# Kernel optimization log

Hardware: AMD Instinct MI355X
Metric: run time of the kernel (lower is better)

The kernel has to match this reference:

```python
import jax, jax.numpy as jnp
import numpy as np

EPS = 1e-06


def setup_inputs() -> dict:
    key = jax.random.key(0)
    k_feat, k_gamma, k_beta = jax.random.split(key, 3)
    N, C, B = 1_000_000, 64, 8
    feat = jax.random.normal(k_feat, (N, C), dtype=jnp.float32)
    # cumulative offsets: 8 equal segments of 125k points, last == N
    offset = (jnp.arange(1, B + 1, dtype=jnp.int64)) * (N // B)
    gamma = jax.random.normal(k_gamma, (1, C), dtype=jnp.float32) * 0.1
    beta = jax.random.normal(k_beta, (1, C), dtype=jnp.float32) * 0.1
    return {"feat": feat, "offset": offset, "gamma": gamma, "beta": beta}


def reference(feat, offset, gamma, beta):
    N, C = feat.shape
    B = offset.shape[0]
    # segment id of each point: first offset strictly greater than index
    batch = jnp.searchsorted(offset, jnp.arange(N), side="right")  # [N]
    # per-segment L2 norm over points, per channel: sqrt(sum feat^2)
    sumsq = jax.ops.segment_sum(feat * feat, batch, num_segments=B)  # [B, C]
    response = jnp.sqrt(sumsq)  # [B, C]
    response_norm = response / (jnp.mean(response, axis=1, keepdims=True) + EPS)  # [B, C]
    # broadcast per-segment channel scale back to points
    out = feat + gamma * (feat * response_norm[batch]) + beta  # [N, C]
    return out
```

## Files before the change

kernel.cpp:

```cpp
#include <hip/hip_runtime.h>
#include <math.h>

#define EPS 1e-6f
#define C_CH 64
#define BPS_A 256
#define BPS_C 256

typedef float f32x4 __attribute__((ext_vector_type(4)));

__global__ __launch_bounds__(256) void sumsq_partial(
    const float4* __restrict__ feat,
    const int* __restrict__ offset,
    float* __restrict__ partial)
{
    const int seg  = blockIdx.x / BPS_A;
    const int bip  = blockIdx.x - seg * BPS_A;
    const int start = (seg == 0) ? 0 : offset[seg - 1];
    const int end   = offset[seg];

    const int t    = threadIdx.x;
    const int c4   = t & 15;
    const int rsub = t >> 4;

    float4 a0 = make_float4(0.f, 0.f, 0.f, 0.f);
    float4 a1 = make_float4(0.f, 0.f, 0.f, 0.f);

    const int stride = BPS_A * 32;
    for (int row = start + bip * 32 + rsub; row < end; row += stride) {
        float4 v = feat[row * 16 + c4];
        a0.x = fmaf(v.x, v.x, a0.x);
        a0.y = fmaf(v.y, v.y, a0.y);
        a0.z = fmaf(v.z, v.z, a0.z);
        a0.w = fmaf(v.w, v.w, a0.w);
        int row2 = row + 16;
        if (row2 < end) {
            float4 w = feat[row2 * 16 + c4];
            a1.x = fmaf(w.x, w.x, a1.x);
            a1.y = fmaf(w.y, w.y, a1.y);
            a1.z = fmaf(w.z, w.z, a1.z);
            a1.w = fmaf(w.w, w.w, a1.w);
        }
    }
    a0.x += a1.x; a0.y += a1.y; a0.z += a1.z; a0.w += a1.w;

    __shared__ float lds[16][C_CH];
    lds[rsub][4 * c4 + 0] = a0.x;
    lds[rsub][4 * c4 + 1] = a0.y;
    lds[rsub][4 * c4 + 2] = a0.z;
    lds[rsub][4 * c4 + 3] = a0.w;
    __syncthreads();

    if (t < C_CH) {
        float s = 0.f;
        #pragma unroll
        for (int r = 0; r < 16; ++r) s += lds[r][t];
        partial[blockIdx.x * C_CH + t] = s;
    }
}

__global__ __launch_bounds__(256) void apply_kernel(
    const float4* __restrict__ feat,
    const int* __restrict__ offset,
    const float* __restrict__ partial,
    const float* __restrict__ gamma,
    const float4* __restrict__ beta4,
    f32x4* __restrict__ out)
{
    const int seg = blockIdx.x / BPS_C;
    const int bip = blockIdx.x - seg * BPS_C;
    const int start = (seg == 0) ? 0 : offset[seg - 1];
    const int end   = offset[seg];

    const int t    = threadIdx.x;
    const int c    = t & 63;
    const int q    = t >> 6;

    __shared__ float red[4][C_CH];
    __shared__ float mulsh[C_CH];

    {
        float s = 0.f;
        const float* p = partial + (seg * BPS_A) * C_CH + c;
        for (int b = q; b < BPS_A; b += 4) s += p[b * C_CH];
        red[q][c] = s;
        __syncthreads();
        if (t < C_CH) {
            float tot  = red[0][c] + red[1][c] + red[2][c] + red[3][c];
            float resp = sqrtf(tot);
            float m = resp;
            #pragma unroll
            for (int off = 1; off < 64; off <<= 1) m += __shfl_xor(m, off, 64);
            float mean = m * (1.0f / 64.0f);
            float rn   = resp / (mean + EPS);
            mulsh[c] = 1.0f + gamma[c] * rn;
        }
        __syncthreads();
    }

    const int c4 = t & 15;
    const int rsub = t >> 4;
    const float4 mm = ((const float4*)mulsh)[c4];
    const float4 bt = beta4[c4];

    const int stride = BPS_C * 32;
    for (int row = start + bip * 32 + rsub; row < end; row += stride) {
        float4 v = feat[row * 16 + c4];
        f32x4 o;
        o.x = fmaf(v.x, mm.x, bt.x);
        o.y = fmaf(v.y, mm.y, bt.y);
        o.z = fmaf(v.z, mm.z, bt.z);
        o.w = fmaf(v.w, mm.w, bt.w);
        __builtin_nontemporal_store(o, &out[row * 16 + c4]);
        int row2 = row + 16;
        if (row2 < end) {
            float4 w = feat[row2 * 16 + c4];
            f32x4 o2;
            o2.x = fmaf(w.x, mm.x, bt.x);
            o2.y = fmaf(w.y, mm.y, bt.y);
            o2.z = fmaf(w.z, mm.z, bt.z);
            o2.w = fmaf(w.w, mm.w, bt.w);
            __builtin_nontemporal_store(o2, &out[row2 * 16 + c4]);
        }
    }
}

extern "C" void kernel_launch(void* const* d_in, const int* in_sizes, int n_in,
                              void* d_out, int out_size, void* d_ws, size_t ws_size,
                              hipStream_t stream)
{
    const float4* feat   = (const float4*)d_in[0];
    const int*    offset = (const int*)d_in[1];
    const float*  gamma  = (const float*)d_in[2];
    const float4* beta4  = (const float4*)d_in[3];
    f32x4*        out    = (f32x4*)d_out;

    const int B = in_sizes[1];

    float* partial = (float*)d_ws;

    sumsq_partial<<<B * BPS_A, 256, 0, stream>>>(feat, offset, partial);
    apply_kernel<<<B * BPS_C, 256, 0, stream>>>(feat, offset, partial,
                                                gamma, beta4, (f32x4*)out);
}
```

Before: 132.9 us.

## Split segments into halves and overlap second-half reduction with first-half apply

Splits the two-pass work into three launches: sum of squares for the first half of segments, then a mixed kernel that reduces the second half while applying the first half, then applying the second half. The goal is to overlap the two phases and keep recently read feature data in the last-level cache before its second read, cutting DRAM traffic. It adds one kernel launch and relies on low-index blocks being dispatched first within the mixed kernel.

New measurement: 142.0 us. +6.8%, slower.

```diff
diff --git a/kernel.cpp b/kernel.cpp
--- a/kernel.cpp
+++ b/kernel.cpp
@@ -8,16 +8,10 @@
 
 typedef float f32x4 __attribute__((ext_vector_type(4)));
 
-__global__ __launch_bounds__(256) void sumsq_partial(
-    const float4* __restrict__ feat,
-    const int* __restrict__ offset,
-    float* __restrict__ partial)
+__device__ __forceinline__ void sumsq_block(
+    const float4* __restrict__ feat, int start, int end, int bip,
+    float* __restrict__ partial_row)
 {
-    const int seg  = blockIdx.x / BPS_A;
-    const int bip  = blockIdx.x - seg * BPS_A;
-    const int start = (seg == 0) ? 0 : offset[seg - 1];
-    const int end   = offset[seg];
-
     const int t    = threadIdx.x;
     const int c4   = t & 15;
     const int rsub = t >> 4;
@@ -54,33 +48,28 @@
         float s = 0.f;
         #pragma unroll
         for (int r = 0; r < 16; ++r) s += lds[r][t];
-        partial[blockIdx.x * C_CH + t] = s;
+        partial_row[t] = s;
     }
 }
 
-__global__ __launch_bounds__(256) void apply_kernel(
+__device__ __forceinline__ void apply_block(
     const float4* __restrict__ feat,
-    const int* __restrict__ offset,
-    const float* __restrict__ partial,
+    const float* __restrict__ partial_seg,
     const float* __restrict__ gamma,
     const float4* __restrict__ beta4,
-    f32x4* __restrict__ out)
+    f32x4* __restrict__ out,
+    int start, int end, int bip)
 {
-    const int seg = blockIdx.x / BPS_C;
-    const int bip = blockIdx.x - seg * BPS_C;
-    const int start = (seg == 0) ? 0 : offset[seg - 1];
-    const int end   = offset[seg];
-
-    const int t    = threadIdx.x;
-    const int c    = t & 63;
-    const int q    = t >> 6;
+    const int t = threadIdx.x;
+    const int c = t & 63;
+    const int q = t >> 6;
 
     __shared__ float red[4][C_CH];
     __shared__ float mulsh[C_CH];
 
     {
         float s = 0.f;
-        const float* p = partial + (seg * BPS_A) * C_CH + c;
+        const float* p = partial_seg + c;
         for (int b = q; b < BPS_A; b += 4) s += p[b * C_CH];
         red[q][c] = s;
         __syncthreads();
@@ -91,13 +80,12 @@
             #pragma unroll
             for (int off = 1; off < 64; off <<= 1) m += __shfl_xor(m, off, 64);
             float mean = m * (1.0f / 64.0f);
-            float rn   = resp / (mean + EPS);
-            mulsh[c] = 1.0f + gamma[c] * rn;
+            mulsh[c] = 1.0f + gamma[c] * (resp / (mean + EPS));
         }
         __syncthreads();
     }
 
-    const int c4 = t & 15;
+    const int c4   = t & 15;
     const int rsub = t >> 4;
     const float4 mm = ((const float4*)mulsh)[c4];
     const float4 bt = beta4[c4];
@@ -124,6 +112,54 @@
     }
 }
 
+__global__ __launch_bounds__(256) void k_sumsq(
+    const float4* __restrict__ feat, const int* __restrict__ offset,
+    float* __restrict__ partial, int segBase)
+{
+    const int seg = segBase + blockIdx.x / BPS_A;
+    const int bip = blockIdx.x % BPS_A;
+    const int start = (seg == 0) ? 0 : offset[seg - 1];
+    const int end   = offset[seg];
+    sumsq_block(feat, start, end, bip, partial + (seg * BPS_A + bip) * C_CH);
+}
+
+__global__ __launch_bounds__(256) void k_mixed(
+    const float4* __restrict__ feat, const int* __restrict__ offset,
+    float* __restrict__ partial, const float* __restrict__ gamma,
+    const float4* __restrict__ beta4, f32x4* __restrict__ out,
+    int h1)
+{
+    const int nA = ((int)gridDim.x - h1 * BPS_C);
+    if ((int)blockIdx.x < nA) {
+        const int seg = h1 + blockIdx.x / BPS_A;
+        const int bip = blockIdx.x % BPS_A;
+        const int start = (seg == 0) ? 0 : offset[seg - 1];
+        const int end   = offset[seg];
+        sumsq_block(feat, start, end, bip, partial + (seg * BPS_A + bip) * C_CH);
+    } else {
+        const int lin = blockIdx.x - nA;
+        const int seg = lin / BPS_C;
+        const int bip = lin % BPS_C;
+        const int start = (seg == 0) ? 0 : offset[seg - 1];
+        const int end   = offset[seg];
+        apply_block(feat, partial + seg * BPS_A * C_CH, gamma, beta4, out,
+                    start, end, bip);
+    }
+}
+
+__global__ __launch_bounds__(256) void k_apply(
+    const float4* __restrict__ feat, const int* __restrict__ offset,
+    const float* __restrict__ partial, const float* __restrict__ gamma,
+    const float4* __restrict__ beta4, f32x4* __restrict__ out, int segBase)
+{
+    const int seg = segBase + blockIdx.x / BPS_C;
+    const int bip = blockIdx.x % BPS_C;
+    const int start = (seg == 0) ? 0 : offset[seg - 1];
+    const int end   = offset[seg];
+    apply_block(feat, partial + seg * BPS_A * C_CH, gamma, beta4, out,
+                start, end, bip);
+}
+
 extern "C" void kernel_launch(void* const* d_in, const int* in_sizes, int n_in,
                               void* d_out, int out_size, void* d_ws, size_t ws_size,
                               hipStream_t stream)
@@ -135,10 +171,20 @@
     f32x4*        out    = (f32x4*)d_out;
 
     const int B = in_sizes[1];
-
     float* partial = (float*)d_ws;
 
-    sumsq_partial<<<B * BPS_A, 256, 0, stream>>>(feat, offset, partial);
-    apply_kernel<<<B * BPS_C, 256, 0, stream>>>(feat, offset, partial,
-                                                gamma, beta4, (f32x4*)out);
+    const int h1 = B / 2;
+    const int h2 = B - h1;
+
+    if (h1 > 0) {
+        k_sumsq<<<h1 * BPS_A, 256, 0, stream>>>(feat, offset, partial, 0);
+        k_mixed<<<h2 * BPS_A + h1 * BPS_C, 256, 0, stream>>>(
+            feat, offset, partial, gamma, beta4, out, h1);
+        k_apply<<<h2 * BPS_C, 256, 0, stream>>>(
+            feat, offset, partial, gamma, beta4, out, h1);
+    } else {
+        k_sumsq<<<BPS_A, 256, 0, stream>>>(feat, offset, partial, 0);
+        k_apply<<<BPS_C, 256, 0, stream>>>(feat, offset, partial, gamma, beta4,
+                                           out, 0);
+    }
 }
```

## Pipeline per-segment sumsq, finalize, and apply across staggered launches

Applied to the files above, without the earlier changes.

Replaces the two whole-tensor kernels with B+2 launches. Launch p computes partial sums for segment p, finalizes the scale for segment p-1, and applies the output to segment p-2. The aim is to reread each segment's features soon after its reduction while they may still be in cache, and to overlap the reduce and apply phases. In exchange it adds about ten launch overheads and smaller grids per launch, and the workspace partial count adapts to ws_size.

Result: slower. 241.1 us (+81.4%).

```diff
diff --git a/kernel.cpp b/kernel.cpp
--- a/kernel.cpp
+++ b/kernel.cpp
@@ -3,123 +3,119 @@
 
 #define EPS 1e-6f
 #define C_CH 64
-#define BPS_A 256
-#define BPS_C 256
+#define NAPPLY 1024
 
 typedef float f32x4 __attribute__((ext_vector_type(4)));
 
-__global__ __launch_bounds__(256) void sumsq_partial(
+__global__ __launch_bounds__(256) void k_phase(
     const float4* __restrict__ feat,
-    const int* __restrict__ offset,
-    float* __restrict__ partial)
+    const int*    __restrict__ offset,
+    float*        __restrict__ partial,
+    float*        __restrict__ muls,
+    const float*  __restrict__ gamma,
+    const float4* __restrict__ beta4,
+    f32x4*        __restrict__ out,
+    int p, int nA, int nS, int R)
 {
-    const int seg  = blockIdx.x / BPS_A;
-    const int bip  = blockIdx.x - seg * BPS_A;
-    const int start = (seg == 0) ? 0 : offset[seg - 1];
-    const int end   = offset[seg];
+    __shared__ float lds[16][C_CH];
 
     const int t    = threadIdx.x;
     const int c4   = t & 15;
     const int rsub = t >> 4;
+    const int bid  = blockIdx.x;
 
-    float4 a0 = make_float4(0.f, 0.f, 0.f, 0.f);
-    float4 a1 = make_float4(0.f, 0.f, 0.f, 0.f);
+    if (bid < nA) {
+        const int seg   = p - 2;
+        const int start = (seg == 0) ? 0 : offset[seg - 1];
+        const int end   = offset[seg];
 
-    const int stride = BPS_A * 32;
-    for (int row = start + bip * 32 + rsub; row < end; row += stride) {
-        float4 v = feat[row * 16 + c4];
-        a0.x = fmaf(v.x, v.x, a0.x);
-        a0.y = fmaf(v.y, v.y, a0.y);
-        a0.z = fmaf(v.z, v.z, a0.z);
-        a0.w = fmaf(v.w, v.w, a0.w);
-        int row2 = row + 16;
-        if (row2 < end) {
-            float4 w = feat[row2 * 16 + c4];
-            a1.x = fmaf(w.x, w.x, a1.x);
-            a1.y = fmaf(w.y, w.y, a1.y);
-            a1.z = fmaf(w.z, w.z, a1.z);
-            a1.w = fmaf(w.w, w.w, a1.w);
+        const float4 mm = ((const float4*)(muls + seg * C_CH))[c4];
+        const float4 bt = beta4[c4];
+
+        const int stride = nA * 32;
+        for (int row = start + bid * 32 + rsub; row < end; row += stride) {
+            float4 v = feat[row * 16 + c4];
+            f32x4 o;
+            o.x = fmaf(v.x, mm.x, bt.x);
+            o.y = fmaf(v.y, mm.y, bt.y);
+            o.z = fmaf(v.z, mm.z, bt.z);
+            o.w = fmaf(v.w, mm.w, bt.w);
+            __builtin_nontemporal_store(o, &out[row * 16 + c4]);
+            int row2 = row + 16;
+            if (row2 < end) {
+                float4 w = feat[row2 * 16 + c4];
+                f32x4 o2;
+                o2.x = fmaf(w.x, mm.x, bt.x);
+                o2.y = fmaf(w.y, mm.y, bt.y);
+                o2.z = fmaf(w.z, mm.z, bt.z);
+                o2.w = fmaf(w.w, mm.w, bt.w);
+                __builtin_nontemporal_store(o2, &out[row2 * 16 + c4]);
+            }
         }
-    }
-    a0.x += a1.x; a0.y += a1.y; a0.z += a1.z; a0.w += a1.w;
+    } else if (bid < nA + nS) {
+        const int seg   = p;
+        const int bip   = bid - nA;
+        const int start = (seg == 0) ? 0 : offset[seg - 1];
+        const int end   = offset[seg];
 
-    __shared__ float lds[16][C_CH];
-    lds[rsub][4 * c4 + 0] = a0.x;
-    lds[rsub][4 * c4 + 1] = a0.y;
-    lds[rsub][4 * c4 + 2] = a0.z;
-    lds[rsub][4 * c4 + 3] = a0.w;
-    __syncthreads();
+        float4 a0 = make_float4(0.f, 0.f, 0.f, 0.f);
+        float4 a1 = make_float4(0.f, 0.f, 0.f, 0.f);
 
-    if (t < C_CH) {
-        float s = 0.f;
-        #pragma unroll
-        for (int r = 0; r < 16; ++r) s += lds[r][t];
-        partial[blockIdx.x * C_CH + t] = s;
-    }
-}
+        const int stride = R * 32;
+        for (int row = start + bip * 32 + rsub; row < end; row += stride) {
+            float4 v = feat[row * 16 + c4];
+            a0.x = fmaf(v.x, v.x, a0.x);
+            a0.y = fmaf(v.y, v.y, a0.y);
+            a0.z = fmaf(v.z, v.z, a0.z);
+            a0.w = fmaf(v.w, v.w, a0.w);
+            int row2 = row + 16;
+            if (row2 < end) {
+                float4 w = feat[row2 * 16 + c4];
+                a1.x = fmaf(w.x, w.x, a1.x);
+                a1.y = fmaf(w.y, w.y, a1.y);
+                a1.z = fmaf(w.z, w.z, a1.z);
+                a1.w = fmaf(w.w, w.w, a1.w);
+            }
+        }
+        a0.x += a1.x; a0.y += a1.y; a0.z += a1.z; a0.w += a1.w;
 
-__global__ __launch_bounds__(256) void apply_kernel(
-    const float4* __restrict__ feat,
-    const int* __restrict__ offset,
-    const float* __restrict__ partial,
-    const float* __restrict__ gamma,
-    const float4* __restrict__ beta4,
-    f32x4* __restrict__ out)
-{
-    const int seg = blockIdx.x / BPS_C;
-    const int bip = blockIdx.x - seg * BPS_C;
-    const int start = (seg == 0) ? 0 : offset[seg - 1];
-    const int end   = offset[seg];
+        lds[rsub][4 * c4 + 0] = a0.x;
+        lds[rsub][4 * c4 + 1] = a0.y;
+        lds[rsub][4 * c4 + 2] = a0.z;
+        lds[rsub][4 * c4 + 3] = a0.w;
+        __syncthreads();
 
-    const int t    = threadIdx.x;
-    const int c    = t & 63;
-    const int q    = t >> 6;
+        if (t < C_CH) {
+            float s = 0.f;
+            #pragma unroll
+            for (int r = 0; r < 16; ++r) s += lds[r][t];
+            partial[(seg * R + bip) * C_CH + t] = s;
+        }
+    } else {
+        const int seg = p - 1;
+        const float* base = partial + seg * R * C_CH;
 
-    __shared__ float red[4][C_CH];
-    __shared__ float mulsh[C_CH];
+        float4 acc = make_float4(0.f, 0.f, 0.f, 0.f);
+        for (int r = rsub; r < R; r += 16) {
+            float4 v = ((const float4*)(base + r * C_CH))[c4];
+            acc.x += v.x; acc.y += v.y; acc.z += v.z; acc.w += v.w;
+        }
+        lds[rsub][4 * c4 + 0] = acc.x;
+        lds[rsub][4 * c4 + 1] = acc.y;
+        lds[rsub][4 * c4 + 2] = acc.z;
+        lds[rsub][4 * c4 + 3] = acc.w;
+        __syncthreads();
 
-    {
-        float s = 0.f;
-        const float* p = partial + (seg * BPS_A) * C_CH + c;
-        for (int b = q; b < BPS_A; b += 4) s += p[b * C_CH];
-        red[q][c] = s;
-        __syncthreads();
         if (t < C_CH) {
-            float tot  = red[0][c] + red[1][c] + red[2][c] + red[3][c];
-            float resp = sqrtf(tot);
+            float s = 0.f;
+            #pragma unroll
+            for (int r = 0; r < 16; ++r) s += lds[r][t];
+            float resp = sqrtf(s);
             float m = resp;
             #pragma unroll
             for (int off = 1; off < 64; off <<= 1) m += __shfl_xor(m, off, 64);
             float mean = m * (1.0f / 64.0f);
-            float rn   = resp / (mean + EPS);
-            mulsh[c] = 1.0f + gamma[c] * rn;
-        }
-        __syncthreads();
-    }
-
-    const int c4 = t & 15;
-    const int rsub = t >> 4;
-    const float4 mm = ((const float4*)mulsh)[c4];
-    const float4 bt = beta4[c4];
-
-    const int stride = BPS_C * 32;
-    for (int row = start + bip * 32 + rsub; row < end; row += stride) {
-        float4 v = feat[row * 16 + c4];
-        f32x4 o;
-        o.x = fmaf(v.x, mm.x, bt.x);
-        o.y = fmaf(v.y, mm.y, bt.y);
-        o.z = fmaf(v.z, mm.z, bt.z);
-        o.w = fmaf(v.w, mm.w, bt.w);
-        __builtin_nontemporal_store(o, &out[row * 16 + c4]);
-        int row2 = row + 16;
-        if (row2 < end) {
-            float4 w = feat[row2 * 16 + c4];
-            f32x4 o2;
-            o2.x = fmaf(w.x, mm.x, bt.x);
-            o2.y = fmaf(w.y, mm.y, bt.y);
-            o2.z = fmaf(w.z, mm.z, bt.z);
-            o2.w = fmaf(w.w, mm.w, bt.w);
-            __builtin_nontemporal_store(o2, &out[row2 * 16 + c4]);
+            muls[seg * C_CH + t] = 1.0f + gamma[t] * (resp / (mean + EPS));
         }
     }
 }
@@ -136,9 +132,20 @@
 
     const int B = in_sizes[1];
 
+    int R = 1024;
+    while ((size_t)B * R * C_CH * 4 + (size_t)B * C_CH * 4 > ws_size && R > 64)
+        R >>= 1;
+
     float* partial = (float*)d_ws;
+    float* muls    = partial + (size_t)B * R * C_CH;
 
-    sumsq_partial<<<B * BPS_A, 256, 0, stream>>>(feat, offset, partial);
-    apply_kernel<<<B * BPS_C, 256, 0, stream>>>(feat, offset, partial,
-                                                gamma, beta4, (f32x4*)out);
+    for (int p = 0; p <= B + 1; ++p) {
+        const int nA   = (p >= 2) ? NAPPLY : 0;
+        const int nS   = (p < B) ? R : 0;
+        const int hasF = (p >= 1 && p <= B) ? 1 : 0;
+        const int grid = nA + nS + hasF;
+        if (grid == 0) continue;
+        k_phase<<<grid, 256, 0, stream>>>(feat, offset, partial, muls,
+                                          gamma, beta4, out, p, nA, nS, R);
+    }
 }
```

## Fuse reduction and apply into one cooperative kernel with grid sync

Applied to the files above, without the earlier changes.

Merges the sum-of-squares pass and the scaling pass into a single cooperative kernel that uses a grid-wide barrier between them, so one launch is removed. The grid is shrunk to 128 blocks per segment (1024 total) so that all blocks can be resident at once. Each block's slice of feat (about 32 KB) can stay in cache for the second pass, which now uses nontemporal loads. The costs are fewer blocks in flight, the grid barrier itself, and a dependence on cooperative-launch residency.

Result: slower. 268.3 us (+101.8%).

```diff
diff --git a/kernel.cpp b/kernel.cpp
--- a/kernel.cpp
+++ b/kernel.cpp
@@ -1,20 +1,27 @@
 #include <hip/hip_runtime.h>
+#include <hip/hip_cooperative_groups.h>
 #include <math.h>
+
+namespace cg = cooperative_groups;
 
 #define EPS 1e-6f
 #define C_CH 64
-#define BPS_A 256
-#define BPS_C 256
+#define RPS  128
 
 typedef float f32x4 __attribute__((ext_vector_type(4)));
 
-__global__ __launch_bounds__(256) void sumsq_partial(
+__global__ __launch_bounds__(256) void fused_kernel(
     const float4* __restrict__ feat,
-    const int* __restrict__ offset,
-    float* __restrict__ partial)
+    const int*    __restrict__ offset,
+    float*        __restrict__ partial,
+    const float*  __restrict__ gamma,
+    const float4* __restrict__ beta4,
+    f32x4*        __restrict__ out)
 {
-    const int seg  = blockIdx.x / BPS_A;
-    const int bip  = blockIdx.x - seg * BPS_A;
+    cg::grid_group grid = cg::this_grid();
+
+    const int seg   = blockIdx.x / RPS;
+    const int bip   = blockIdx.x % RPS;
     const int start = (seg == 0) ? 0 : offset[seg - 1];
     const int end   = offset[seg];
 
@@ -22,66 +29,55 @@
     const int c4   = t & 15;
     const int rsub = t >> 4;
 
-    float4 a0 = make_float4(0.f, 0.f, 0.f, 0.f);
-    float4 a1 = make_float4(0.f, 0.f, 0.f, 0.f);
-
-    const int stride = BPS_A * 32;
-    for (int row = start + bip * 32 + rsub; row < end; row += stride) {
-        float4 v = feat[row * 16 + c4];
-        a0.x = fmaf(v.x, v.x, a0.x);
-        a0.y = fmaf(v.y, v.y, a0.y);
-        a0.z = fmaf(v.z, v.z, a0.z);
-        a0.w = fmaf(v.w, v.w, a0.w);
-        int row2 = row + 16;
-        if (row2 < end) {
-            float4 w = feat[row2 * 16 + c4];
-            a1.x = fmaf(w.x, w.x, a1.x);
-            a1.y = fmaf(w.y, w.y, a1.y);
-            a1.z = fmaf(w.z, w.z, a1.z);
-            a1.w = fmaf(w.w, w.w, a1.w);
-        }
-    }
-    a0.x += a1.x; a0.y += a1.y; a0.z += a1.z; a0.w += a1.w;
-
     __shared__ float lds[16][C_CH];
-    lds[rsub][4 * c4 + 0] = a0.x;
-    lds[rsub][4 * c4 + 1] = a0.y;
-    lds[rsub][4 * c4 + 2] = a0.z;
-    lds[rsub][4 * c4 + 3] = a0.w;
-    __syncthreads();
-
-    if (t < C_CH) {
-        float s = 0.f;
-        #pragma unroll
-        for (int r = 0; r < 16; ++r) s += lds[r][t];
-        partial[blockIdx.x * C_CH + t] = s;
-    }
-}
-
-__global__ __launch_bounds__(256) void apply_kernel(
-    const float4* __restrict__ feat,
-    const int* __restrict__ offset,
-    const float* __restrict__ partial,
-    const float* __restrict__ gamma,
-    const float4* __restrict__ beta4,
-    f32x4* __restrict__ out)
-{
-    const int seg = blockIdx.x / BPS_C;
-    const int bip = blockIdx.x - seg * BPS_C;
-    const int start = (seg == 0) ? 0 : offset[seg - 1];
-    const int end   = offset[seg];
-
-    const int t    = threadIdx.x;
-    const int c    = t & 63;
-    const int q    = t >> 6;
-
     __shared__ float red[4][C_CH];
     __shared__ float mulsh[C_CH];
 
     {
+        float4 a0 = make_float4(0.f, 0.f, 0.f, 0.f);
+        float4 a1 = make_float4(0.f, 0.f, 0.f, 0.f);
+
+        const int stride = RPS * 32;
+        for (int row = start + bip * 32 + rsub; row < end; row += stride) {
+            float4 v = feat[row * 16 + c4];
+            a0.x = fmaf(v.x, v.x, a0.x);
+            a0.y = fmaf(v.y, v.y, a0.y);
+            a0.z = fmaf(v.z, v.z, a0.z);
+            a0.w = fmaf(v.w, v.w, a0.w);
+            int row2 = row + 16;
+            if (row2 < end) {
+                float4 w = feat[row2 * 16 + c4];
+                a1.x = fmaf(w.x, w.x, a1.x);
+                a1.y = fmaf(w.y, w.y, a1.y);
+                a1.z = fmaf(w.z, w.z, a1.z);
+                a1.w = fmaf(w.w, w.w, a1.w);
+            }
+        }
+        a0.x += a1.x; a0.y += a1.y; a0.z += a1.z; a0.w += a1.w;
+
+        lds[rsub][4 * c4 + 0] = a0.x;
+        lds[rsub][4 * c4 + 1] = a0.y;
+        lds[rsub][4 * c4 + 2] = a0.z;
+        lds[rsub][4 * c4 + 3] = a0.w;
+        __syncthreads();
+
+        if (t < C_CH) {
+            float s = 0.f;
+            #pragma unroll
+            for (int r = 0; r < 16; ++r) s += lds[r][t];
+            partial[(seg * RPS + bip) * C_CH + t] = s;
+        }
+    }
+
+    __threadfence();
+    grid.sync();
+
+    {
+        const int c = t & 63;
+        const int q = t >> 6;
         float s = 0.f;
-        const float* p = partial + (seg * BPS_A) * C_CH + c;
-        for (int b = q; b < BPS_A; b += 4) s += p[b * C_CH];
+        const float* p = partial + seg * RPS * C_CH + c;
+        for (int b = q; b < RPS; b += 4) s += p[b * C_CH];
         red[q][c] = s;
         __syncthreads();
         if (t < C_CH) {
@@ -91,35 +87,35 @@
             #pragma unroll
             for (int off = 1; off < 64; off <<= 1) m += __shfl_xor(m, off, 64);
             float mean = m * (1.0f / 64.0f);
-            float rn   = resp / (mean + EPS);
-            mulsh[c] = 1.0f + gamma[c] * rn;
+            mulsh[c] = 1.0f + gamma[c] * (resp / (mean + EPS));
         }
         __syncthreads();
     }
 
-    const int c4 = t & 15;
-    const int rsub = t >> 4;
-    const float4 mm = ((const float4*)mulsh)[c4];
-    const float4 bt = beta4[c4];
+    {
+        const float4 mm = ((const float4*)mulsh)[c4];
+        const float4 bt = beta4[c4];
+        const f32x4* featv = (const f32x4*)feat;
 
-    const int stride = BPS_C * 32;
-    for (int row = start + bip * 32 + rsub; row < end; row += stride) {
-        float4 v = feat[row * 16 + c4];
-        f32x4 o;
-        o.x = fmaf(v.x, mm.x, bt.x);
-        o.y = fmaf(v.y, mm.y, bt.y);
-        o.z = fmaf(v.z, mm.z, bt.z);
-        o.w = fmaf(v.w, mm.w, bt.w);
-        __builtin_nontemporal_store(o, &out[row * 16 + c4]);
-        int row2 = row + 16;
-        if (row2 < end) {
-            float4 w = feat[row2 * 16 + c4];
-            f32x4 o2;
-            o2.x = fmaf(w.x, mm.x, bt.x);
-            o2.y = fmaf(w.y, mm.y, bt.y);
-            o2.z = fmaf(w.z, mm.z, bt.z);
-            o2.w = fmaf(w.w, mm.w, bt.w);
-            __builtin_nontemporal_store(o2, &out[row2 * 16 + c4]);
+        const int stride = RPS * 32;
+        for (int row = start + bip * 32 + rsub; row < end; row += stride) {
+            f32x4 v = __builtin_nontemporal_load(&featv[row * 16 + c4]);
+            f32x4 o;
+            o.x = fmaf(v.x, mm.x, bt.x);
+            o.y = fmaf(v.y, mm.y, bt.y);
+            o.z = fmaf(v.z, mm.z, bt.z);
+            o.w = fmaf(v.w, mm.w, bt.w);
+            __builtin_nontemporal_store(o, &out[row * 16 + c4]);
+            int row2 = row + 16;
+            if (row2 < end) {
+                f32x4 w = __builtin_nontemporal_load(&featv[row2 * 16 + c4]);
+                f32x4 o2;
+                o2.x = fmaf(w.x, mm.x, bt.x);
+                o2.y = fmaf(w.y, mm.y, bt.y);
+                o2.z = fmaf(w.z, mm.z, bt.z);
+                o2.w = fmaf(w.w, mm.w, bt.w);
+                __builtin_nontemporal_store(o2, &out[row2 * 16 + c4]);
+            }
         }
     }
 }
@@ -135,10 +131,13 @@
     f32x4*        out    = (f32x4*)d_out;
 
     const int B = in_sizes[1];
-
     float* partial = (float*)d_ws;
 
-    sumsq_partial<<<B * BPS_A, 256, 0, stream>>>(feat, offset, partial);
-    apply_kernel<<<B * BPS_C, 256, 0, stream>>>(feat, offset, partial,
-                                                gamma, beta4, (f32x4*)out);
+    void* args[] = {
+        (void*)&feat, (void*)&offset, (void*)&partial,
+        (void*)&gamma, (void*)&beta4, (void*)&out
+    };
+    hipLaunchCooperativeKernel((void*)fused_kernel,
+                               dim3(B * RPS), dim3(256),
+                               args, 0, stream);
 }
```
